# Kernel tuning notes

Hardware: AMD Instinct MI355X
Metric: run time of the kernel (lower is better)

The kernel has to match this reference:

```python
import jax, jax.numpy as jnp
from jax import lax
import numpy as np

KSIZE = 3
SCALE = 2
SOFTMAX_SCALE = 10.0
EPS = 1e-4  # escape_NaN buffer


def prelu(x, a):
    return jnp.where(x >= 0, x, a * x)


def conv1x1(x, W, b):
    # x: [B,C,H,W], W: [O,C]
    return jnp.einsum('bchw,oc->bohw', x, W) + b[None, :, None, None]


def extract_patches(x, k, s):
    """torch.nn.Unfold with 'same' padding. x: [B,C,H,W] -> [B, L, C, k, k],
    L = ceil(H/s)*ceil(W/s), patches row-major, channel ordering (C, kh, kw)."""
    B, C, H, W = x.shape
    Ho, Wo = -(-H // s), -(-W // s)
    ph = max(0, (Ho - 1) * s + k - H)
    pw = max(0, (Wo - 1) * s + k - W)
    xp = jnp.pad(x, ((0, 0), (0, 0), (ph // 2, ph - ph // 2), (pw // 2, pw - pw // 2)))
    # small fixed k*k loop (<=36), each slice is strided view -> [B,C,Ho,Wo]
    sl = [xp[:, :, i:i + s * (Ho - 1) + 1:s, j:j + s * (Wo - 1) + 1:s]
          for i in range(k) for j in range(k)]
    p = jnp.stack(sl, axis=2).reshape(B, C, k, k, Ho, Wo)
    return p.transpose(0, 4, 5, 1, 2, 3).reshape(B, Ho * Wo, C, k, k)


def reference(x, W1, b1, a1, W2, b2, a2, Wa, ba, aa, Wd, bd):
    B, C, H, W = x.shape
    s, k = SCALE, KSIZE
    kernel = s * k  # 6
    # H, W divisible by s -> reflect mod-pad is a no-op
    embed_w = prelu(conv1x1(x, Wa, ba), aa)      # [B,64,H,W]
    match_in = prelu(conv1x1(x, W1, b1), a1)     # [B,32,H,W]

    # assembly patches: kernel=6, stride=2, same padding -> L = (H/2)*(W/2)
    raw_w = extract_patches(embed_w, kernel, s)  # [B,L,64,6,6]

    # bilinear 1/s downsample (align_corners=False, scale=1/2) == 2x2 mean pool
    ref = x.reshape(B, C, H // s, s, W // s, s).mean(axis=(3, 5))
    ref = prelu(conv1x1(ref, W2, b2), a2)        # [B,32,H/2,W/2]

    w = extract_patches(ref, k, 1)               # [B,L,32,3,3]
    norm = jnp.maximum(jnp.sqrt(jnp.sum(w * w, axis=(2, 3, 4), keepdims=True)), EPS)
    wn = (w / norm).reshape(B, -1, (C // 2) * k * k)          # [B,L,288]

    xp = extract_patches(match_in, k, 1).reshape(B, -1, (C // 2) * k * k)  # [B,H*W,288]
    # per-sample dynamic conv == correlation of query patches with ref patches
    yi = jnp.einsum('blc,bqc->blq', wn, xp)      # [B, L, H*W]
    yi = jax.nn.softmax(yi * SOFTMAX_SCALE, axis=1)
    L = (H // s) * (W // s)
    yi = yi.reshape(B, L, H, W)

    # per-sample conv_transpose2d(yi, raw_w, stride=s*stride=2, padding=s=2)
    def tconv(y, wk):  # y: [L,H,W], wk: [L,64,6,6]
        wf = jnp.flip(wk, axis=(-2, -1)).transpose(1, 0, 2, 3)  # [64,L,6,6]
        pad = kernel - 1 - s  # 3
        return lax.conv_general_dilated(
            y[None], wf, (1, 1), ((pad, pad), (pad, pad)), lhs_dilation=(s, s),
            dimension_numbers=('NCHW', 'OIHW', 'NCHW'))[0]

    yt = jax.vmap(tconv)(yi, raw_w)              # [B,64,2H,2W]

    # self.down: 3x3 conv, stride 2, pad 1
    yd = lax.conv_general_dilated(yt, Wd, (2, 2), ((1, 1), (1, 1)),
                                  dimension_numbers=('NCHW', 'OIHW', 'NCHW'))
    yd = yd + bd[None, :, None, None]
    return (yd / 6.0)[:, :, :H, :W]


def setup_inputs() -> dict:
    key = jax.random.key(0)
    ks = jax.random.split(key, 8)
    B, C, H, W = 2, 64, 96, 96
    Cr = C // 2
    return {
        'x': jax.random.normal(ks[0], (B, C, H, W), jnp.float32),
        'W1': jax.random.normal(ks[1], (Cr, C), jnp.float32) * 0.1,
        'b1': jnp.zeros((Cr,), jnp.float32),
        'a1': jnp.full((1,), 0.25, jnp.float32),
        'W2': jax.random.normal(ks[2], (Cr, C), jnp.float32) * 0.1,
        'b2': jnp.zeros((Cr,), jnp.float32),
        'a2': jnp.full((1,), 0.25, jnp.float32),
        'Wa': jax.random.normal(ks[3], (C, C), jnp.float32) * 0.1,
        'ba': jnp.zeros((C,), jnp.float32),
        'aa': jnp.full((1,), 0.25, jnp.float32),
        'Wd': jax.random.normal(ks[4], (C, C, 3, 3), jnp.float32) * 0.05,
        'bd': jnp.zeros((C,), jnp.float32),
    }
```

## Files before the change

### kernel.cpp

```cpp
#include <hip/hip_runtime.h>

typedef _Float16 half8 __attribute__((ext_vector_type(8)));
typedef float float4v __attribute__((ext_vector_type(4)));


__global__ __launch_bounds__(256) void conv_embed_match(
    const float* __restrict__ x, const float* __restrict__ Wa, const float* __restrict__ ba,
    const float* __restrict__ aa, const float* __restrict__ W1, const float* __restrict__ b1,
    const float* __restrict__ a1, float* __restrict__ embed2, float* __restrict__ match2) {
    int b = blockIdx.z;
    const float* xb = x + (size_t)b * 64 * 9216;
    int p = blockIdx.x * 256 + threadIdx.x;
    int chunk = blockIdx.y;
    float xin[64];
#pragma unroll
    for (int ci = 0; ci < 64; ++ci) xin[ci] = xb[ci * 9216 + p];
    bool isE = chunk < 4;
    int co0 = (isE ? chunk : chunk - 4) * 16;
    const float* W = isE ? Wa : W1;
    const float* bb = isE ? ba : b1;
    float alpha = (isE ? aa : a1)[0];
    float* dst = isE ? (embed2 + (size_t)b * 64 * 9216) : (match2 + (size_t)b * 32 * 9216);
#pragma unroll
    for (int c = 0; c < 16; ++c) {
        int co = co0 + c;
        float s = bb[co];
#pragma unroll
        for (int ci = 0; ci < 64; ++ci) s += W[co * 64 + ci] * xin[ci];
        dst[co * 9216 + p] = s >= 0.f ? s : alpha * s;
    }
}

__global__ __launch_bounds__(256) void conv_ref_pooled(
    const float* __restrict__ x, const float* __restrict__ W2, const float* __restrict__ b2,
    const float* __restrict__ a2, float* __restrict__ refb2) {
    int b = blockIdx.z;
    const float* xb = x + (size_t)b * 64 * 9216;
    int p = blockIdx.x * 256 + threadIdx.x;
    int ph = p / 48, pw = p % 48;
    int co0 = blockIdx.y * 16;
    float xin[64];
#pragma unroll
    for (int ci = 0; ci < 64; ++ci) {
        const float* q = xb + ci * 9216 + ph * 2 * 96 + pw * 2;
        xin[ci] = 0.25f * (q[0] + q[1] + q[96] + q[97]);
    }
    float alpha = a2[0];
    float* dst = refb2 + (size_t)b * 32 * 2304;
#pragma unroll
    for (int c = 0; c < 16; ++c) {
        int co = co0 + c;
        float s = b2[co];
#pragma unroll
        for (int ci = 0; ci < 64; ++ci) s += W2[co * 64 + ci] * xin[ci];
        dst[co * 2304 + p] = s >= 0.f ? s : alpha * s;
    }
}


__global__ __launch_bounds__(256) void build_xp(const float* __restrict__ match,
                                                _Float16* __restrict__ xp) {
    int q = blockIdx.x * 4 + (threadIdx.x >> 6);
    int lane = threadIdx.x & 63;
    int qh = q / 96, qw = q % 96;
#pragma unroll
    for (int t = 0; t < 5; ++t) {
        int k = lane + t * 64;
        if (k < 288) {
            int c = k / 9, r = k % 9;
            int y = qh + r / 3 - 1, x = qw + r % 3 - 1;
            float v = (y >= 0 && y < 96 && x >= 0 && x < 96) ? match[c * 9216 + y * 96 + x] : 0.f;
            xp[(size_t)q * 288 + k] = (_Float16)v;
        }
    }
}

__global__ void build_wn(const float* __restrict__ ref, _Float16* __restrict__ wn) {
    int l = blockIdx.x;
    int oh = l / 48, ow = l % 48;
    int lane = threadIdx.x;
    float vals[5];
    float ss = 0.f;
#pragma unroll
    for (int t = 0; t < 5; ++t) {
        int i = lane + t * 64;
        float v = 0.f;
        if (i < 288) {
            int c = i / 9, r = i % 9, kh = r / 3, kw = r % 3;
            int y = oh + kh - 1, x = ow + kw - 1;
            v = (y >= 0 && y < 48 && x >= 0 && x < 48) ? ref[c * 2304 + y * 48 + x] : 0.f;
        }
        vals[t] = v;
        ss += v * v;
    }
#pragma unroll
    for (int d = 32; d; d >>= 1) ss += __shfl_xor(ss, d);
    float norm = sqrtf(ss);
    norm = norm < 1e-4f ? 1e-4f : norm;
    float inv = 10.f / norm;
#pragma unroll
    for (int t = 0; t < 5; ++t) {
        int i = lane + t * 64;
        if (i < 288) wn[(size_t)l * 288 + i] = (_Float16)(vals[t] * inv);
    }
}

__global__ void build_Wt(const float* __restrict__ embed, _Float16* __restrict__ Wt) {
    int idx = blockIdx.x * 256 + threadIdx.x;
    if (idx >= 2304 * 2304) return;
    int row = idx / 2304, l = idx % 2304;
    int o = row / 36, rem = row % 36, i = rem / 6, j = rem % 6;
    int lh = l / 48, lw = l % 48;
    int y = 2 * lh + i - 2, x = 2 * lw + j - 2;
    float v = (y >= 0 && y < 96 && x >= 0 && x < 96) ? embed[o * 9216 + y * 96 + x] : 0.f;
    Wt[idx] = (_Float16)v;
}

__global__ __launch_bounds__(256) void softmax_rows(const float* __restrict__ S,
                                                    _Float16* __restrict__ yi) {
    int q = blockIdx.x;
    const float* row = S + (size_t)q * 2304;
    int tid = threadIdx.x;
    float v[9];
    float m = -1e30f;
#pragma unroll
    for (int t = 0; t < 9; ++t) {
        v[t] = row[tid + t * 256];
        m = fmaxf(m, v[t]);
    }
    __shared__ float red[8];
#pragma unroll
    for (int d = 32; d; d >>= 1) m = fmaxf(m, __shfl_xor(m, d));
    if ((tid & 63) == 0) red[tid >> 6] = m;
    __syncthreads();
    m = fmaxf(fmaxf(red[0], red[1]), fmaxf(red[2], red[3]));
    float s = 0.f;
#pragma unroll
    for (int t = 0; t < 9; ++t) {
        v[t] = expf(v[t] - m);
        s += v[t];
    }
#pragma unroll
    for (int d = 32; d; d >>= 1) s += __shfl_xor(s, d);
    __syncthreads();
    if ((tid & 63) == 0) red[(tid >> 6) + 4] = s;
    __syncthreads();
    s = red[4] + red[5] + red[6] + red[7];
    float inv = 1.f / s;
    _Float16* orow = yi + (size_t)q * 2304;
#pragma unroll
    for (int t = 0; t < 9; ++t) orow[tid + t * 256] = (_Float16)(v[t] * inv);
}

template <int MODE>
__global__ __launch_bounds__(256) void gemm16(const _Float16* __restrict__ A,
                                              const _Float16* __restrict__ B, int M, int N, int K,
                                              void* __restrict__ outv,
                                              const float* __restrict__ bias) {
    __shared__ _Float16 As[128 * 32];
    __shared__ _Float16 Bs[128 * 32];
    int tid = threadIdx.x;
    int wave = tid >> 6, lane = tid & 63;
    int wm = wave >> 1, wn_ = wave & 1;
    int quad = lane >> 4, mrow = lane & 15;
    int m0 = blockIdx.y * 128, n0 = blockIdx.x * 128;
    int lrow = lane >> 2, lslot = lane & 3;
    float4v acc[4][4] = {};

    for (int k0 = 0; k0 < K; k0 += 32) {
#pragma unroll
        for (int r = 0; r < 2; ++r) {
            int c = wave * 2 + r;
            int row = c * 16 + lrow;
            int cc = lslot ^ ((row >> 1) & 3);
            const _Float16* ga = A + (size_t)(m0 + row) * K + k0 + cc * 8;
            const _Float16* gb = B + (size_t)(n0 + row) * K + k0 + cc * 8;
            __builtin_amdgcn_global_load_lds(
                (const __attribute__((address_space(1))) unsigned int*)ga,
                (__attribute__((address_space(3))) unsigned int*)&As[c * 512], 16, 0, 0);
            __builtin_amdgcn_global_load_lds(
                (const __attribute__((address_space(1))) unsigned int*)gb,
                (__attribute__((address_space(3))) unsigned int*)&Bs[c * 512], 16, 0, 0);
        }
        __syncthreads();
        half8 af[4], bf[4];
#pragma unroll
        for (int t = 0; t < 4; ++t) {
            int arow = wm * 64 + t * 16 + mrow;
            af[t] = *(const half8*)&As[arow * 32 + (quad ^ ((arow >> 1) & 3)) * 8];
            int brow = wn_ * 64 + t * 16 + mrow;
            bf[t] = *(const half8*)&Bs[brow * 32 + (quad ^ ((brow >> 1) & 3)) * 8];
        }
#pragma unroll
        for (int i = 0; i < 4; ++i)
#pragma unroll
            for (int j = 0; j < 4; ++j)
                acc[i][j] = __builtin_amdgcn_mfma_f32_16x16x32_f16(af[i], bf[j], acc[i][j], 0, 0, 0);
        __syncthreads();
    }

#pragma unroll
    for (int i = 0; i < 4; ++i)
#pragma unroll
        for (int j = 0; j < 4; ++j)
#pragma unroll
            for (int r = 0; r < 4; ++r) {
                int row = m0 + wm * 64 + i * 16 + quad * 4 + r;
                int col = n0 + wn_ * 64 + j * 16 + mrow;
                float v = acc[i][j][r];
                if (MODE == 0) {
                    ((float*)outv)[(size_t)row * N + col] = v;
                } else if (MODE == 1) {
                    ((_Float16*)outv)[(size_t)row * N + col] = (_Float16)v;
                } else {
                    if (row < 64)
                        ((float*)outv)[(size_t)row * N + col] = (v + bias[row]) * (1.f / 6.f);
                }
            }
}


__global__ void gather_yt(const _Float16* __restrict__ Z, _Float16* __restrict__ yth) {
    int idx = blockIdx.x * 256 + threadIdx.x;
    if (idx >= 64 * 192 * 192) return;
    int o = idx / 36864, r = idx % 36864, Y = r / 192, X = r % 192;
    float s = 0.f;
    for (int i = Y & 1; i < 6; i += 2) {
        int h2 = Y + 2 - i;
        if (h2 < 0) continue;
        int h = h2 >> 1;
        if (h >= 96) continue;
        for (int j = X & 1; j < 6; j += 2) {
            int w2 = X + 2 - j;
            if (w2 < 0) continue;
            int w = w2 >> 1;
            if (w >= 96) continue;
            s += (float)Z[(size_t)(o * 36 + i * 6 + j) * 9216 + h * 96 + w];
        }
    }
    yth[idx] = (_Float16)s;
}

__global__ __launch_bounds__(256) void build_P(const _Float16* __restrict__ yth,
                                               _Float16* __restrict__ P) {
    int q = blockIdx.x * 4 + (threadIdx.x >> 6);
    int lane = threadIdx.x & 63;
    int y = q / 96, x = q % 96;
#pragma unroll
    for (int t = 0; t < 9; ++t) {
        int k = lane + t * 64;
        int o = k / 9, r = k % 9;
        int Y = 2 * y - 1 + r / 3, X = 2 * x - 1 + r % 3;
        _Float16 v = (_Float16)0.f;
        if (Y >= 0 && Y < 192 && X >= 0 && X < 192) v = yth[o * 36864 + Y * 192 + X];
        P[(size_t)q * 576 + k] = v;
    }
}

__global__ void build_Wdh(const float* __restrict__ Wd, _Float16* __restrict__ Wdh) {
    int idx = blockIdx.x * 256 + threadIdx.x;
    if (idx >= 128 * 576) return;
    int op = idx / 576;
    Wdh[idx] = (_Float16)(op < 64 ? Wd[idx] : 0.f);
}


extern "C" void kernel_launch(void* const* d_in, const int* in_sizes, int n_in,
                              void* d_out, int out_size, void* d_ws, size_t ws_size,
                              hipStream_t stream) {
    const float* x = (const float*)d_in[0];
    const float* W1 = (const float*)d_in[1];
    const float* b1 = (const float*)d_in[2];
    const float* a1 = (const float*)d_in[3];
    const float* W2 = (const float*)d_in[4];
    const float* b2 = (const float*)d_in[5];
    const float* a2 = (const float*)d_in[6];
    const float* Wa = (const float*)d_in[7];
    const float* ba = (const float*)d_in[8];
    const float* aa = (const float*)d_in[9];
    const float* Wd = (const float*)d_in[10];
    const float* bd = (const float*)d_in[11];
    float* out = (float*)d_out;

    char* ws = (char*)d_ws;
    float* S = (float*)ws;           ws += 84934656;
    _Float16* yi = (_Float16*)ws;    ws += 42467328;
    _Float16* Wt = (_Float16*)ws;    ws += 10616832;
    _Float16* xp = (_Float16*)ws;    ws += 5308416;
    _Float16* wn = (_Float16*)ws;    ws += 1327104;
    float* embed2 = (float*)ws;      ws += 4718592;
    float* match2 = (float*)ws;      ws += 2359296;
    float* refb2 = (float*)ws;       ws += 589824;
    _Float16* Wdh = (_Float16*)ws;   ws += 147456;
    _Float16* Z = (_Float16*)S;
    _Float16* P = yi;
    _Float16* yth = Wt;

    build_Wdh<<<288, 256, 0, stream>>>(Wd, Wdh);
    conv_embed_match<<<dim3(36, 6, 2), 256, 0, stream>>>(x, Wa, ba, aa, W1, b1, a1, embed2, match2);
    conv_ref_pooled<<<dim3(9, 2, 2), 256, 0, stream>>>(x, W2, b2, a2, refb2);

    for (int b = 0; b < 2; ++b) {
        float* outb = out + (size_t)b * 64 * 9216;
        const float* embed = embed2 + (size_t)b * 64 * 9216;
        const float* match = match2 + (size_t)b * 32 * 9216;
        const float* refb = refb2 + (size_t)b * 32 * 2304;

        build_xp<<<2304, 256, 0, stream>>>(match, xp);
        build_wn<<<2304, 64, 0, stream>>>(refb, wn);
        build_Wt<<<20736, 256, 0, stream>>>(embed, Wt);

        gemm16<0><<<dim3(18, 72), 256, 0, stream>>>(xp, wn, 9216, 2304, 288, S, nullptr);
        softmax_rows<<<9216, 256, 0, stream>>>(S, yi);

        gemm16<1><<<dim3(72, 18), 256, 0, stream>>>(Wt, yi, 2304, 9216, 2304, Z, nullptr);

        gather_yt<<<9216, 256, 0, stream>>>(Z, yth);
        build_P<<<2304, 256, 0, stream>>>(yth, P);
        gemm16<2><<<dim3(72, 1), 256, 0, stream>>>(Wdh, P, 128, 9216, 576, outb, bd);
    }
}
```

Measured before the change: 638.8 us.

## Use BK=64 GEMM tiles, fp16 score matrix, and swapped grid order

The GEMM kernel now stages a K-depth of 64 per iteration with an 8-way XOR swizzle, which halves the number of barrier-separated iterations and doubles the MFMA work between syncs. The patch matrices are padded from 288 to 320 columns with zeros so K divides evenly. The similarity matrix S is written and read as fp16 instead of fp32, cutting its write and softmax read traffic in half, but pre-softmax logits lose precision. The large second GEMM also gets a swapped block-index mapping, which changes the order in which tiles are scheduled.

```diff
diff --git a/kernel.cpp b/kernel.cpp
--- a/kernel.cpp
+++ b/kernel.cpp
@@ -66,12 +66,13 @@
 #pragma unroll
     for (int t = 0; t < 5; ++t) {
         int k = lane + t * 64;
+        float v = 0.f;
         if (k < 288) {
             int c = k / 9, r = k % 9;
             int y = qh + r / 3 - 1, x = qw + r % 3 - 1;
-            float v = (y >= 0 && y < 96 && x >= 0 && x < 96) ? match[c * 9216 + y * 96 + x] : 0.f;
-            xp[(size_t)q * 288 + k] = (_Float16)v;
+            if (y >= 0 && y < 96 && x >= 0 && x < 96) v = match[c * 9216 + y * 96 + x];
         }
+        xp[(size_t)q * 320 + k] = (_Float16)v;
     }
 }
 
@@ -101,7 +102,7 @@
 #pragma unroll
     for (int t = 0; t < 5; ++t) {
         int i = lane + t * 64;
-        if (i < 288) wn[(size_t)l * 288 + i] = (_Float16)(vals[t] * inv);
+        wn[(size_t)l * 320 + i] = (_Float16)(i < 288 ? vals[t] * inv : 0.f);
     }
 }
 
@@ -116,16 +117,16 @@
     Wt[idx] = (_Float16)v;
 }
 
-__global__ __launch_bounds__(256) void softmax_rows(const float* __restrict__ S,
+__global__ __launch_bounds__(256) void softmax_rows(const _Float16* __restrict__ S16,
                                                     _Float16* __restrict__ yi) {
     int q = blockIdx.x;
-    const float* row = S + (size_t)q * 2304;
+    const _Float16* row = S16 + (size_t)q * 2304;
     int tid = threadIdx.x;
     float v[9];
     float m = -1e30f;
 #pragma unroll
     for (int t = 0; t < 9; ++t) {
-        v[t] = row[tid + t * 256];
+        v[t] = (float)row[tid + t * 256];
         m = fmaxf(m, v[t]);
     }
     __shared__ float red[8];
@@ -152,29 +153,31 @@
     for (int t = 0; t < 9; ++t) orow[tid + t * 256] = (_Float16)(v[t] * inv);
 }
 
-template <int MODE>
-__global__ __launch_bounds__(256) void gemm16(const _Float16* __restrict__ A,
-                                              const _Float16* __restrict__ B, int M, int N, int K,
-                                              void* __restrict__ outv,
-                                              const float* __restrict__ bias) {
-    __shared__ _Float16 As[128 * 32];
-    __shared__ _Float16 Bs[128 * 32];
+template <int MODE, int MSWAP>
+__global__ __launch_bounds__(256) void gemm_bk64(const _Float16* __restrict__ A,
+                                                 const _Float16* __restrict__ B,
+                                                 int M, int N, int K,
+                                                 void* __restrict__ outv,
+                                                 const float* __restrict__ bias) {
+    __shared__ _Float16 As[128 * 64];
+    __shared__ _Float16 Bs[128 * 64];
     int tid = threadIdx.x;
     int wave = tid >> 6, lane = tid & 63;
     int wm = wave >> 1, wn_ = wave & 1;
     int quad = lane >> 4, mrow = lane & 15;
-    int m0 = blockIdx.y * 128, n0 = blockIdx.x * 128;
-    int lrow = lane >> 2, lslot = lane & 3;
+    int m0 = (MSWAP ? blockIdx.x : blockIdx.y) * 128;
+    int n0 = (MSWAP ? blockIdx.y : blockIdx.x) * 128;
+    int crow = lane >> 3, cslot = lane & 7;
     float4v acc[4][4] = {};
 
-    for (int k0 = 0; k0 < K; k0 += 32) {
-#pragma unroll
-        for (int r = 0; r < 2; ++r) {
-            int c = wave * 2 + r;
-            int row = c * 16 + lrow;
-            int cc = lslot ^ ((row >> 1) & 3);
-            const _Float16* ga = A + (size_t)(m0 + row) * K + k0 + cc * 8;
-            const _Float16* gb = B + (size_t)(n0 + row) * K + k0 + cc * 8;
+    for (int k0 = 0; k0 < K; k0 += 64) {
+#pragma unroll
+        for (int r = 0; r < 4; ++r) {
+            int c = wave * 4 + r;
+            int row = c * 8 + crow;
+            int ss = cslot ^ (row & 7);
+            const _Float16* ga = A + (size_t)(m0 + row) * K + k0 + ss * 8;
+            const _Float16* gb = B + (size_t)(n0 + row) * K + k0 + ss * 8;
             __builtin_amdgcn_global_load_lds(
                 (const __attribute__((address_space(1))) unsigned int*)ga,
                 (__attribute__((address_space(3))) unsigned int*)&As[c * 512], 16, 0, 0);
@@ -183,19 +186,24 @@
                 (__attribute__((address_space(3))) unsigned int*)&Bs[c * 512], 16, 0, 0);
         }
         __syncthreads();
-        half8 af[4], bf[4];
-#pragma unroll
-        for (int t = 0; t < 4; ++t) {
-            int arow = wm * 64 + t * 16 + mrow;
-            af[t] = *(const half8*)&As[arow * 32 + (quad ^ ((arow >> 1) & 3)) * 8];
-            int brow = wn_ * 64 + t * 16 + mrow;
-            bf[t] = *(const half8*)&Bs[brow * 32 + (quad ^ ((brow >> 1) & 3)) * 8];
-        }
-#pragma unroll
-        for (int i = 0; i < 4; ++i)
-#pragma unroll
-            for (int j = 0; j < 4; ++j)
-                acc[i][j] = __builtin_amdgcn_mfma_f32_16x16x32_f16(af[i], bf[j], acc[i][j], 0, 0, 0);
+        half8 af[2][4], bf[2][4];
+#pragma unroll
+        for (int d = 0; d < 2; ++d)
+#pragma unroll
+            for (int t = 0; t < 4; ++t) {
+                int ar = wm * 64 + t * 16 + mrow;
+                af[d][t] = *(const half8*)&As[ar * 64 + (((d * 4 + quad) ^ (ar & 7)) * 8)];
+                int br = wn_ * 64 + t * 16 + mrow;
+                bf[d][t] = *(const half8*)&Bs[br * 64 + (((d * 4 + quad) ^ (br & 7)) * 8)];
+            }
+#pragma unroll
+        for (int d = 0; d < 2; ++d)
+#pragma unroll
+            for (int i = 0; i < 4; ++i)
+#pragma unroll
+                for (int j = 0; j < 4; ++j)
+                    acc[i][j] =
+                        __builtin_amdgcn_mfma_f32_16x16x32_f16(af[d][i], bf[d][j], acc[i][j], 0, 0, 0);
         __syncthreads();
     }
 
@@ -208,9 +216,7 @@
                 int row = m0 + wm * 64 + i * 16 + quad * 4 + r;
                 int col = n0 + wn_ * 64 + j * 16 + mrow;
                 float v = acc[i][j][r];
-                if (MODE == 0) {
-                    ((float*)outv)[(size_t)row * N + col] = v;
-                } else if (MODE == 1) {
+                if (MODE == 1) {
                     ((_Float16*)outv)[(size_t)row * N + col] = (_Float16)v;
                 } else {
                     if (row < 64)
@@ -283,16 +289,17 @@
     float* out = (float*)d_out;
 
     char* ws = (char*)d_ws;
-    float* S = (float*)ws;           ws += 84934656;
+    char* sreg = ws;                 ws += 84934656;
     _Float16* yi = (_Float16*)ws;    ws += 42467328;
     _Float16* Wt = (_Float16*)ws;    ws += 10616832;
-    _Float16* xp = (_Float16*)ws;    ws += 5308416;
-    _Float16* wn = (_Float16*)ws;    ws += 1327104;
+    _Float16* xp = (_Float16*)ws;    ws += 5898240;
+    _Float16* wn = (_Float16*)ws;    ws += 1474560;
     float* embed2 = (float*)ws;      ws += 4718592;
     float* match2 = (float*)ws;      ws += 2359296;
     float* refb2 = (float*)ws;       ws += 589824;
     _Float16* Wdh = (_Float16*)ws;   ws += 147456;
-    _Float16* Z = (_Float16*)S;
+    _Float16* S16 = (_Float16*)sreg;
+    _Float16* Z = (_Float16*)sreg;
     _Float16* P = yi;
     _Float16* yth = Wt;
 
@@ -310,13 +317,13 @@
         build_wn<<<2304, 64, 0, stream>>>(refb, wn);
         build_Wt<<<20736, 256, 0, stream>>>(embed, Wt);
 
-        gemm16<0><<<dim3(18, 72), 256, 0, stream>>>(xp, wn, 9216, 2304, 288, S, nullptr);
-        softmax_rows<<<9216, 256, 0, stream>>>(S, yi);
-
-        gemm16<1><<<dim3(72, 18), 256, 0, stream>>>(Wt, yi, 2304, 9216, 2304, Z, nullptr);
+        gemm_bk64<1, 0><<<dim3(18, 72), 256, 0, stream>>>(xp, wn, 9216, 2304, 320, S16, nullptr);
+        softmax_rows<<<9216, 256, 0, stream>>>(S16, yi);
+
+        gemm_bk64<1, 1><<<dim3(18, 72), 256, 0, stream>>>(Wt, yi, 2304, 9216, 2304, Z, nullptr);
 
         gather_yt<<<9216, 256, 0, stream>>>(Z, yth);
         build_P<<<2304, 256, 0, stream>>>(yth, P);
-        gemm16<2><<<dim3(72, 1), 256, 0, stream>>>(Wdh, P, 128, 9216, 576, outb, bd);
-    }
-}
+        gemm_bk64<2, 0><<<dim3(72, 1), 256, 0, stream>>>(Wdh, P, 128, 9216, 576, outb, bd);
+    }
+}
```

Result: faster. 615.7 us (-3.6%).
